# Performance work log

Hardware: AMD Instinct MI355X
Metric: run time of the kernel (lower is better)

Reference implementation:

```python
import jax, jax.numpy as jnp
import numpy as np

N_NODES = 15
K = 5
L_IN = 1920
C_OUT = 256
L3 = L_IN - 3 * K + 3  # 1908
EPS = 1e-5


def setup_inputs() -> dict:
    key = jax.random.key(0)
    ks = jax.random.split(key, 18)
    B, E = 128, 56
    s = 0.05
    inp = {
        'X': jax.random.normal(ks[0], (B, N_NODES, L_IN), jnp.float32),
        'edge_index': jax.random.randint(ks[1], (2, E), 0, N_NODES),
        'edge_weight': jax.random.uniform(ks[2], (E,), jnp.float32),
        # grouped conv params (groups = N_NODES): per-group channels 1->16->32->1
        'conv1_w': jax.random.normal(ks[3], (16 * N_NODES, 1, K), jnp.float32) * s,
        'conv1_b': jnp.zeros((16 * N_NODES,), jnp.float32),
        'conv2_w': jax.random.normal(ks[4], (32 * N_NODES, 16, K), jnp.float32) * s,
        'conv2_b': jnp.zeros((32 * N_NODES,), jnp.float32),
        'conv3_w': jax.random.normal(ks[5], (N_NODES, 32, K), jnp.float32) * s,
        'conv3_b': jnp.zeros((N_NODES,), jnp.float32),
        # GCNConv: lin weight [out,in] + bias
        'gcn_w': jax.random.normal(ks[6], (C_OUT, L3), jnp.float32) * s,
        'gcn_b': jnp.zeros((C_OUT,), jnp.float32),
        'lin1_w': jax.random.normal(ks[7], (C_OUT, L_IN), jnp.float32) * s,
        'lin1_b': jnp.zeros((C_OUT,), jnp.float32),
        # GraphNorm params
        'gn_w': jnp.ones((C_OUT,), jnp.float32),
        'gn_b': jnp.zeros((C_OUT,), jnp.float32),
        'gn_ms': jnp.ones((C_OUT,), jnp.float32),
        'out_w': jax.random.normal(ks[8], (16, C_OUT), jnp.float32) * s,
        'out_b': jnp.zeros((16,), jnp.float32),
    }
    return inp


def _gconv(x, w, b):
    # grouped valid conv1d, NCH layout
    y = jax.lax.conv_general_dilated(
        x, w, window_strides=(1,), padding='VALID',
        dimension_numbers=('NCH', 'OIH', 'NCH'),
        feature_group_count=N_NODES)
    return y + b[None, :, None]


def _gcn(x, edge_index, edge_weight, W, b):
    # x: [B, N, L3]; batched GCNConv with shared edge structure (no per-t loop)
    src, dst = edge_index[0], edge_index[1]
    loop = jnp.arange(N_NODES)
    src = jnp.concatenate([src, loop])
    dst = jnp.concatenate([dst, loop])
    ew = jnp.concatenate([edge_weight, jnp.ones((N_NODES,), edge_weight.dtype)])
    deg = jnp.zeros((N_NODES,), ew.dtype).at[dst].add(ew)  # in-degree on target
    dinv = jnp.where(deg > 0, jax.lax.rsqrt(deg), 0.0)
    norm = dinv[src] * ew * dinv[dst]  # [E']
    xl = jnp.einsum('bnf,of->bno', x, W)  # [B, N, C_OUT]
    msg = norm[None, :, None] * xl[:, src, :]  # [B, E', C_OUT]
    out = jnp.zeros_like(xl).at[:, dst, :].add(msg)
    return out + b


def reference(X, edge_index, edge_weight, conv1_w, conv1_b, conv2_w, conv2_b,
              conv3_w, conv3_b, gcn_w, gcn_b, lin1_w, lin1_b, gn_w, gn_b,
              gn_ms, out_w, out_b):
    h = jax.nn.leaky_relu(_gconv(X, conv1_w, conv1_b), 0.01)
    h = jax.nn.leaky_relu(_gconv(h, conv2_w, conv2_b), 0.01)
    h = jax.nn.leaky_relu(_gconv(h, conv3_w, conv3_b), 0.01)  # [B, N, L3]
    T = _gcn(h, edge_index, edge_weight, gcn_w, gcn_b)  # [B, N, C_OUT]
    # GraphNorm with batch=None -> single graph over dim 0
    mean = T.mean(axis=0, keepdims=True)
    out = T - mean * gn_ms
    var = (out * out).mean(axis=0, keepdims=True)
    T = gn_w * out / jnp.sqrt(var + EPS) + gn_b
    T = jax.nn.elu(T + jnp.einsum('bnl,ol->bno', X, lin1_w) + lin1_b)
    output = T.mean(axis=1)  # global_mean_pool over nodes -> [B, C_OUT]
    class_output = output @ out_w.T + out_b  # [B, 16]
    return (output, class_output)
```

## Files before the change

kernel.cpp:

```cpp
#include <hip/hip_runtime.h>

typedef unsigned short u16;
typedef unsigned int   u32;

typedef short shortx8   __attribute__((ext_vector_type(8)));
typedef float floatx4   __attribute__((ext_vector_type(4)));
typedef float floatx16  __attribute__((ext_vector_type(16)));
typedef u32   uintx4    __attribute__((ext_vector_type(4)));

typedef u32     u32a     __attribute__((may_alias));
typedef uintx4  uintx4a  __attribute__((may_alias));
typedef shortx8 shortx8a __attribute__((may_alias));

__device__ __forceinline__ u16 f2bf(float f){
  union { float f; u32 i; } v; v.f = f;
  return (u16)((v.i + 0x7fffu + ((v.i >> 16) & 1u)) >> 16);
}
__device__ __forceinline__ u16 f2bf_fast(float f){
  union { float f; u32 i; } v; v.f = f;
  return (u16)((v.i + 0x8000u) >> 16);
}
__device__ __forceinline__ u32 pack2(float lo, float hi){
  union { float f; u32 i; } a, b; a.f = lo; b.f = hi;
  return __builtin_amdgcn_perm(b.i + 0x8000u, a.i + 0x8000u, 0x07060302u);
}
__device__ __forceinline__ u32 cvtpk2(float lo, float hi){
#if __has_builtin(__builtin_amdgcn_cvt_pk_bf16_f32)
  auto pv = __builtin_amdgcn_cvt_pk_bf16_f32(lo, hi);
  if constexpr (sizeof(pv) == 4){
    u32 out; __builtin_memcpy(&out, &pv, 4); return out;
  } else {
    return pack2(lo, hi);
  }
#else
  return pack2(lo, hi);
#endif
}
__device__ __forceinline__ float lrelu(float v){ return fmaxf(v, 0.01f*v); }

__global__ void __launch_bounds__(512, 4) fused_conv(
    const float* __restrict__ X,
    const float* __restrict__ w1, const float* __restrict__ b1,
    const float* __restrict__ w2, const float* __restrict__ b2,
    const float* __restrict__ w3, const float* __restrict__ b3,
    u16* __restrict__ h3p, u16* __restrict__ Xb,
    const float* __restrict__ lw, u16* __restrict__ lwb,
    const float* __restrict__ gw, u16* __restrict__ gwp){
  const int tid  = threadIdx.x;
  const int node = blockIdx.z;
  const int p    = blockIdx.x * 60;
  const int b0   = blockIdx.y * 16;

  __shared__ __attribute__((aligned(16))) u16 sH1[8*1632];
  __shared__ __attribute__((aligned(16))) u16 sH2[8*2720];
  __shared__ __attribute__((aligned(16))) u16 sW2f[2560];
  __shared__ __attribute__((aligned(16))) u16 sW3f[160];
  __shared__ u16 sXb[16*76];
  __shared__ float sW1[80], sB1[16], sB2[32];

  {
    const int bid = blockIdx.x + 32*(blockIdx.y + 8*blockIdx.z);
    if (tid < 256){
      int gid = bid*256 + tid;
      if (gid < 491520){
        lwb[gid] = f2bf(lw[gid]);
      } else {
        int g2 = gid - 491520;
        int row = g2 / 1920;
        int col = g2 - row*1920;
        gwp[g2] = (col < 1908) ? f2bf(gw[row*1908 + col]) : (u16)0;
      }
    }
  }

  {
    const int bls = tid >> 5, i0 = tid & 31;
    const float* xrow = X  + (size_t)((b0 + bls)*15 + node)*1920;
    u16*        xbrow = Xb + (size_t)((b0 + bls)*15 + node)*1920;
    #pragma unroll
    for (int u = 0; u < 3; ++u){
      int i = i0 + 32*u;
      if (i < 76){
        int g = p + i;
        float xv = (i < 72 && g < 1920) ? xrow[g] : 0.f;
        u16 xb = f2bf_fast(xv);
        sXb[bls*76 + i] = xb;
        if (i < 60) xbrow[g] = xb;
      }
    }
    #pragma unroll
    for (int u = 0; u < 5; ++u){
      int d = tid + 512*u;
      int j = d & 7, oc = (d >> 3) & 31, h = (d >> 8) & 1, tap = d >> 9;
      sW2f[d] = f2bf(w2[node*2560 + (oc*16 + h*8 + j)*5 + tap]);
    }
    if (tid < 160){
      int icc = tid / 5, tp = tid - 5*icc;
      sW3f[tp*32 + icc] = f2bf(w3[node*160 + tid]);
    }
    if (tid < 80) sW1[tid] = w1[node*80 + tid];
    if (tid < 16) sB1[tid] = b1[node*16 + tid];
    if (tid < 32) sB2[tid] = b2[node*32 + tid];
  }
  __syncthreads();

  const int w = tid >> 6, lane = tid & 63;
  const int m = lane & 15, quad = lane >> 4;
  const int t32 = lane & 31, h = lane >> 5;

  shortx8 a2t[5];
  #pragma unroll
  for (int tap = 0; tap < 5; ++tap)
    a2t[tap] = *(const shortx8a*)&sW2f[((tap*2 + h)*32 + t32)*8];

  float biasr[16];
  #pragma unroll
  for (int r = 0; r < 16; ++r)
    biasr[r] = sB2[(r&3) + 8*(r>>2) + 4*h];

  shortx8 a3[5];
  {
    const shortx8 zv = {0,0,0,0,0,0,0,0};
    #pragma unroll
    for (int tp = 0; tp < 5; ++tp){
      shortx8 t = *(const shortx8a*)&sW3f[tp*32 + quad*8];
      a3[tp] = (m == 0) ? t : zv;
    }
  }
  const float b3v = b3[node];

  u16* h1w = sH1 + w*1632;
  u16* h2w = sH2 + w*2720;
  for (int i = lane; i < 160; i += 64) h2w[2560 + i] = 0;

  const int c1ic = (lane & 7)*2, c1t0 = (lane >> 3)*9;
  float wa[5], wb[5];
  #pragma unroll
  for (int k = 0; k < 5; ++k){ wa[k] = sW1[c1ic*5 + k]; wb[k] = sW1[c1ic*5 + 5 + k]; }
  const float ba = sB1[c1ic], bbv = sB1[c1ic + 1];

  for (int bb = 0; bb < 2; ++bb){
    const int bl = w + bb*8;

    {
      const u16* xr = sXb + bl*76;
      union { u32 i; float f; } cv;
      float xw[5];
      #pragma unroll
      for (int k = 0; k < 4; ++k){ cv.i = ((u32)xr[c1t0+k]) << 16; xw[k] = cv.f; }
      #pragma unroll
      for (int i = 0; i < 9; ++i){
        const int t = c1t0 + i;
        cv.i = ((u32)xr[t + 4]) << 16; xw[4] = cv.f;
        float va = ba  + wa[0]*xw[0] + wa[1]*xw[1] + wa[2]*xw[2] + wa[3]*xw[3] + wa[4]*xw[4];
        float vb = bbv + wb[0]*xw[0] + wb[1]*xw[1] + wb[2]*xw[2] + wb[3]*xw[3] + wb[4]*xw[4];
        va = lrelu(va); vb = lrelu(vb);
        if (t < 68) *(u32a*)(h1w + t*24 + c1ic) = cvtpk2(va, vb);
        xw[0] = xw[1]; xw[1] = xw[2]; xw[2] = xw[3]; xw[3] = xw[4];
      }
    }
    __syncthreads();

    #pragma unroll
    for (int nt = 0; nt < 2; ++nt){
      const int t0 = nt*32;
      floatx16 acc;
      #pragma unroll
      for (int r = 0; r < 16; ++r) acc[r] = biasr[r];
      #pragma unroll
      for (int tap = 0; tap < 5; ++tap){
        shortx8 bfr = *(const shortx8a*)(h1w + (t0 + t32 + tap)*24 + h*8);
        acc = __builtin_amdgcn_mfma_f32_32x32x16_bf16(a2t[tap], bfr, acc, 0, 0, 0);
      }
      u16* dst = h2w + (t0 + t32)*40;
      #pragma unroll
      for (int r = 0; r < 16; r += 2){
        float v0 = lrelu(acc[r]);
        float v1 = lrelu(acc[r+1]);
        const int oc0 = (r&3) + 8*(r>>2) + 4*h;
        *(u32a*)(dst + oc0) = cvtpk2(v0, v1);
      }
    }
    __syncthreads();

    const int rg = (b0 + bl)*15 + node;
    #pragma unroll
    for (int nt = 0; nt < 4; ++nt){
      floatx4 acc3 = {0.f,0.f,0.f,0.f};
      if (lane < 16) acc3[0] = b3v;
      #pragma unroll
      for (int tp = 0; tp < 5; ++tp){
        shortx8 bfr = *(const shortx8a*)(h2w + (nt*16 + m + tp)*40 + quad*8);
        acc3 = __builtin_amdgcn_mfma_f32_16x16x32_bf16(a3[tp], bfr, acc3, 0, 0, 0);
      }
      const int tl = nt*16 + lane;
      if (lane < 16 && tl < 60){
        const int t3 = p + tl;
        float v = lrelu(acc3[0]);
        h3p[(size_t)rg*1920 + t3] = (t3 < 1908) ? f2bf_fast(v) : (u16)0;
      }
    }
  }
}

__global__ void __launch_bounds__(256) gemm_nt(
    const u16* __restrict__ A0, const u16* __restrict__ B0, float* __restrict__ O0,
    const u16* __restrict__ A1, const u16* __restrict__ B1, float* __restrict__ O1,
    float* __restrict__ gZ){
  const int job = blockIdx.z;
  const u16* A; const u16* Bm; float* O;
  if (job == 0){ A = A0; Bm = B0; O = O0; } else { A = A1; Bm = B1; O = O1; }
  __shared__ __attribute__((aligned(16))) u16 sA[64*88];
  __shared__ __attribute__((aligned(16))) u16 sB[64*88];
  const int tid = threadIdx.x;
  if (blockIdx.x == 0 && blockIdx.y == 0 && job == 0){
    #pragma unroll
    for (int u = 0; u < 30; ++u) gZ[tid + 256*u] = 0.f;
  }
  const int m0 = blockIdx.x*64, n0 = blockIdx.y*64;
  const int row = tid >> 2, kc = tid & 3;
  const int w = tid >> 6, lane = tid & 63;
  const int m = lane & 15, quad = lane >> 4;
  const int mo = (w & 1)*32, no = (w >> 1)*32;
  floatx4 acc[2][2];
  #pragma unroll
  for (int i = 0; i < 2; ++i)
    #pragma unroll
    for (int j = 0; j < 2; ++j)
      #pragma unroll
      for (int r = 0; r < 4; ++r) acc[i][j][r] = 0.f;

  const u16* ap = A  + (size_t)(m0 + row)*1920 + kc*8;
  const u16* bp = Bm + (size_t)(n0 + row)*1920 + kc*8;
  for (int kt = 0; kt < 30; ++kt){
    uintx4 va0 = *(const uintx4a*)ap;
    uintx4 va1 = *(const uintx4a*)(ap + 32);
    uintx4 vb0 = *(const uintx4a*)bp;
    uintx4 vb1 = *(const uintx4a*)(bp + 32);
    ap += 64; bp += 64;
    *(uintx4a*)&sA[row*88 + kc*8]      = va0;
    *(uintx4a*)&sA[row*88 + 32 + kc*8] = va1;
    *(uintx4a*)&sB[row*88 + kc*8]      = vb0;
    *(uintx4a*)&sB[row*88 + 32 + kc*8] = vb1;
    __syncthreads();
    #pragma unroll
    for (int ks = 0; ks < 64; ks += 32){
      const shortx8 af0 = *(const shortx8a*)&sA[(mo      + m)*88 + ks + quad*8];
      const shortx8 af1 = *(const shortx8a*)&sA[(mo + 16 + m)*88 + ks + quad*8];
      const shortx8 bf0 = *(const shortx8a*)&sB[(no      + m)*88 + ks + quad*8];
      const shortx8 bf1 = *(const shortx8a*)&sB[(no + 16 + m)*88 + ks + quad*8];
      acc[0][0] = __builtin_amdgcn_mfma_f32_16x16x32_bf16(af0, bf0, acc[0][0], 0, 0, 0);
      acc[0][1] = __builtin_amdgcn_mfma_f32_16x16x32_bf16(af0, bf1, acc[0][1], 0, 0, 0);
      acc[1][0] = __builtin_amdgcn_mfma_f32_16x16x32_bf16(af1, bf0, acc[1][0], 0, 0, 0);
      acc[1][1] = __builtin_amdgcn_mfma_f32_16x16x32_bf16(af1, bf1, acc[1][1], 0, 0, 0);
    }
    __syncthreads();
  }
  #pragma unroll
  for (int mi = 0; mi < 2; ++mi)
    #pragma unroll
    for (int ni = 0; ni < 2; ++ni)
      #pragma unroll
      for (int r = 0; r < 4; ++r){
        int rr = m0 + mo + mi*16 + quad*4 + r;
        int cc = n0 + no + ni*16 + m;
        O[(size_t)rr*256 + cc] = acc[mi][ni][r];
      }
}

__global__ void __launch_bounds__(256) gcn_agg(
    const float* __restrict__ xl, const int* __restrict__ ei,
    const float* __restrict__ ew, const float* __restrict__ gcn_b,
    float* __restrict__ Tpre, float* __restrict__ gS, float* __restrict__ gS2){
  const int b = blockIdx.x, tid = threadIdx.x;
  __shared__ float sxl[15*256];
  __shared__ float s_deg[15], s_dinv[15], s_norm[71];
  __shared__ int   s_cnt[15], s_start[16], s_fill[15], s_srcl[71];
  if (tid < 15){ s_deg[tid] = 0.f; s_cnt[tid] = 0; s_fill[tid] = 0; }
  #pragma unroll
  for (int n = 0; n < 15; ++n)
    sxl[n*256 + tid] = xl[(size_t)(b*15 + n)*256 + tid];
  __syncthreads();
  int se = 0, de = 0; float we = 0.f;
  if (tid < 71){
    if (tid < 56){ se = ei[tid]; de = ei[56 + tid]; we = ew[tid]; }
    else         { se = tid - 56; de = tid - 56; we = 1.0f; }
    atomicAdd(&s_deg[de], we);
    atomicAdd(&s_cnt[de], 1);
  }
  __syncthreads();
  if (tid < 15) s_dinv[tid] = s_deg[tid] > 0.f ? rsqrtf(s_deg[tid]) : 0.f;
  if (tid == 0){
    int a = 0;
    for (int n = 0; n < 15; ++n){ s_start[n] = a; a += s_cnt[n]; }
    s_start[15] = a;
  }
  __syncthreads();
  if (tid < 71){
    float nrm = s_dinv[se]*we*s_dinv[de];
    int pos = s_start[de] + atomicAdd(&s_fill[de], 1);
    s_srcl[pos] = se; s_norm[pos] = nrm;
  }
  __syncthreads();
  const float gb = gcn_b[tid];
  for (int n = 0; n < 15; ++n){
    float acc = gb;
    const int e0 = s_start[n], e1 = s_start[n+1];
    for (int idx = e0; idx < e1; ++idx)
      acc += s_norm[idx]*sxl[s_srcl[idx]*256 + tid];
    Tpre[(size_t)(b*15 + n)*256 + tid] = acc;
    atomicAdd(&gS [n*256 + tid], acc);
    atomicAdd(&gS2[n*256 + tid], acc*acc);
  }
}

__global__ void __launch_bounds__(256) finalize_k(
    const float* __restrict__ Tpre, const float* __restrict__ l1,
    const float* __restrict__ gS, const float* __restrict__ gS2,
    const float* __restrict__ gn_ms, const float* __restrict__ gn_w,
    const float* __restrict__ gn_b, const float* __restrict__ lin1_b,
    const float* __restrict__ out_w, const float* __restrict__ out_b,
    float* __restrict__ dout){
  const int b = blockIdx.x, tid = threadIdx.x;
  __shared__ float spool[256], spart[256];
  const float gnb = gn_b[tid], lb = lin1_b[tid];
  const float gms = gn_ms[tid], gwc = gn_w[tid];
  float acc = 0.f;
  #pragma unroll
  for (int n = 0; n < 15; ++n){
    const float s  = gS [n*256 + tid];
    const float s2 = gS2[n*256 + tid];
    const float mean = s*(1.f/128.f);
    const float mo   = mean*gms;
    float var = s2*(1.f/128.f) - 2.f*mo*mean + mo*mo;
    var = fmaxf(var, 0.f);
    const float scal = gwc*rsqrtf(var + 1e-5f);
    float t = (Tpre[(size_t)(b*15 + n)*256 + tid] - mo)*scal
              + gnb + l1[(size_t)(b*15 + n)*256 + tid] + lb;
    t = t > 0.f ? t : (__expf(t) - 1.f);
    acc += t;
  }
  const float pool = acc*(1.f/15.f);
  dout[b*256 + tid] = pool;
  spool[tid] = pool;
  __syncthreads();
  const int j = tid >> 4, q = tid & 15;
  float s = 0.f;
  for (int i = 0; i < 16; ++i){
    int cc = q + i*16;
    s += spool[cc]*out_w[j*256 + cc];
  }
  spart[tid] = s;
  __syncthreads();
  if (tid < 16){
    float tot = out_b[tid];
    #pragma unroll
    for (int i = 0; i < 16; ++i) tot += spart[tid*16 + i];
    dout[32768 + b*16 + tid] = tot;
  }
}

extern "C" void kernel_launch(void* const* d_in, const int* in_sizes, int n_in,
                              void* d_out, int out_size, void* d_ws, size_t ws_size,
                              hipStream_t stream){
  (void)in_sizes; (void)n_in; (void)out_size; (void)ws_size;
  const float* X    = (const float*)d_in[0];
  const int*   ei   = (const int*)d_in[1];
  const float* ew   = (const float*)d_in[2];
  const float* w1   = (const float*)d_in[3];
  const float* b1   = (const float*)d_in[4];
  const float* w2   = (const float*)d_in[5];
  const float* b2   = (const float*)d_in[6];
  const float* w3   = (const float*)d_in[7];
  const float* b3   = (const float*)d_in[8];
  const float* gw   = (const float*)d_in[9];
  const float* gb   = (const float*)d_in[10];
  const float* lw   = (const float*)d_in[11];
  const float* lb   = (const float*)d_in[12];
  const float* gnw  = (const float*)d_in[13];
  const float* gnb  = (const float*)d_in[14];
  const float* gnms = (const float*)d_in[15];
  const float* ow   = (const float*)d_in[16];
  const float* ob   = (const float*)d_in[17];

  char* ws = (char*)d_ws;
  u16*   h3p  = (u16*)(ws + 0);
  u16*   gwp  = (u16*)(ws + 7372800);
  u16*   Xb   = (u16*)(ws + 8355840);
  u16*   lwb  = (u16*)(ws + 15728640);
  float* xl   = (float*)(ws + 16711680);
  float* l1   = (float*)(ws + 18677760);
  float* gS   = (float*)(ws + 20643840);
  float* gS2  = (float*)(ws + 20659200);
  float* Tpre = (float*)(ws + 0);

  fused_conv<<<dim3(32, 8, 15), dim3(512), 0, stream>>>(X, w1, b1, w2, b2, w3, b3,
                                                        h3p, Xb, lw, lwb, gw, gwp);
  gemm_nt   <<<dim3(30, 4, 2),  dim3(256), 0, stream>>>(Xb, lwb, l1, h3p, gwp, xl, gS);
  gcn_agg   <<<dim3(128),       dim3(256), 0, stream>>>(xl, ei, ew, gb, Tpre, gS, gS2);
  finalize_k<<<dim3(128),       dim3(256), 0, stream>>>(Tpre, l1, gS, gS2,
                                                        gnms, gnw, gnb, lb, ow, ob,
                                                        (float*)d_out);
}
```

Before: 205.5 us.

## Pair waves per batch row to halve shared scratch and raise occupancy

```diff
diff --git a/kernel.cpp b/kernel.cpp
--- a/kernel.cpp
+++ b/kernel.cpp
@@ -38,7 +38,7 @@
 }
 __device__ __forceinline__ float lrelu(float v){ return fmaxf(v, 0.01f*v); }
 
-__global__ void __launch_bounds__(512, 4) fused_conv(
+__global__ void __launch_bounds__(512, 6) fused_conv(
     const float* __restrict__ X,
     const float* __restrict__ w1, const float* __restrict__ b1,
     const float* __restrict__ w2, const float* __restrict__ b2,
@@ -51,8 +51,8 @@
   const int p    = blockIdx.x * 60;
   const int b0   = blockIdx.y * 16;
 
-  __shared__ __attribute__((aligned(16))) u16 sH1[8*1632];
-  __shared__ __attribute__((aligned(16))) u16 sH2[8*2720];
+  __shared__ __attribute__((aligned(16))) u16 sH1[4*1632];
+  __shared__ __attribute__((aligned(16))) u16 sH2[4*2720];
   __shared__ __attribute__((aligned(16))) u16 sW2f[2560];
   __shared__ __attribute__((aligned(16))) u16 sW3f[160];
   __shared__ u16 sXb[16*76];
@@ -91,8 +91,8 @@
     #pragma unroll
     for (int u = 0; u < 5; ++u){
       int d = tid + 512*u;
-      int j = d & 7, oc = (d >> 3) & 31, h = (d >> 8) & 1, tap = d >> 9;
-      sW2f[d] = f2bf(w2[node*2560 + (oc*16 + h*8 + j)*5 + tap]);
+      int j = d & 7, oc = (d >> 3) & 31, kh = (d >> 8) & 1, tap = d >> 9;
+      sW2f[d] = f2bf(w2[node*2560 + (oc*16 + kh*8 + j)*5 + tap]);
     }
     if (tid < 160){
       int icc = tid / 5, tp = tid - 5*icc;
@@ -105,18 +105,19 @@
   __syncthreads();
 
   const int w = tid >> 6, lane = tid & 63;
+  const int pw = w >> 1, ph = w & 1;
   const int m = lane & 15, quad = lane >> 4;
-  const int t32 = lane & 31, h = lane >> 5;
+  const int t32 = lane & 31, kh = lane >> 5;
 
   shortx8 a2t[5];
   #pragma unroll
   for (int tap = 0; tap < 5; ++tap)
-    a2t[tap] = *(const shortx8a*)&sW2f[((tap*2 + h)*32 + t32)*8];
+    a2t[tap] = *(const shortx8a*)&sW2f[((tap*2 + kh)*32 + t32)*8];
 
   float biasr[16];
   #pragma unroll
   for (int r = 0; r < 16; ++r)
-    biasr[r] = sB2[(r&3) + 8*(r>>2) + 4*h];
+    biasr[r] = sB2[(r&3) + 8*(r>>2) + 4*kh];
 
   shortx8 a3[5];
   {
@@ -129,28 +130,30 @@
   }
   const float b3v = b3[node];
 
-  u16* h1w = sH1 + w*1632;
-  u16* h2w = sH2 + w*2720;
-  for (int i = lane; i < 160; i += 64) h2w[2560 + i] = 0;
-
-  const int c1ic = (lane & 7)*2, c1t0 = (lane >> 3)*9;
+  u16* h1w = sH1 + pw*1632;
+  u16* h2w = sH2 + pw*2720;
+  for (int i = lane + ph*64; i < 160; i += 128) h2w[2560 + i] = 0;
+
+  const int c1ic = (lane & 7)*2;
+  const int cc   = (lane >> 3) + ph*8;
+  const int t0c  = cc*5;
   float wa[5], wb[5];
   #pragma unroll
   for (int k = 0; k < 5; ++k){ wa[k] = sW1[c1ic*5 + k]; wb[k] = sW1[c1ic*5 + 5 + k]; }
   const float ba = sB1[c1ic], bbv = sB1[c1ic + 1];
 
-  for (int bb = 0; bb < 2; ++bb){
-    const int bl = w + bb*8;
-
-    {
+  for (int bb = 0; bb < 4; ++bb){
+    const int bl = pw + bb*4;
+
+    if (t0c < 68){
       const u16* xr = sXb + bl*76;
       union { u32 i; float f; } cv;
       float xw[5];
       #pragma unroll
-      for (int k = 0; k < 4; ++k){ cv.i = ((u32)xr[c1t0+k]) << 16; xw[k] = cv.f; }
-      #pragma unroll
-      for (int i = 0; i < 9; ++i){
-        const int t = c1t0 + i;
+      for (int k = 0; k < 4; ++k){ cv.i = ((u32)xr[t0c+k]) << 16; xw[k] = cv.f; }
+      #pragma unroll
+      for (int i = 0; i < 5; ++i){
+        const int t = t0c + i;
         cv.i = ((u32)xr[t + 4]) << 16; xw[4] = cv.f;
         float va = ba  + wa[0]*xw[0] + wa[1]*xw[1] + wa[2]*xw[2] + wa[3]*xw[3] + wa[4]*xw[4];
         float vb = bbv + wb[0]*xw[0] + wb[1]*xw[1] + wb[2]*xw[2] + wb[3]*xw[3] + wb[4]*xw[4];
@@ -161,15 +164,14 @@
     }
     __syncthreads();
 
-    #pragma unroll
-    for (int nt = 0; nt < 2; ++nt){
-      const int t0 = nt*32;
+    {
+      const int t0 = ph*32;
       floatx16 acc;
       #pragma unroll
       for (int r = 0; r < 16; ++r) acc[r] = biasr[r];
       #pragma unroll
       for (int tap = 0; tap < 5; ++tap){
-        shortx8 bfr = *(const shortx8a*)(h1w + (t0 + t32 + tap)*24 + h*8);
+        shortx8 bfr = *(const shortx8a*)(h1w + (t0 + t32 + tap)*24 + kh*8);
         acc = __builtin_amdgcn_mfma_f32_32x32x16_bf16(a2t[tap], bfr, acc, 0, 0, 0);
       }
       u16* dst = h2w + (t0 + t32)*40;
@@ -177,7 +179,7 @@
       for (int r = 0; r < 16; r += 2){
         float v0 = lrelu(acc[r]);
         float v1 = lrelu(acc[r+1]);
-        const int oc0 = (r&3) + 8*(r>>2) + 4*h;
+        const int oc0 = (r&3) + 8*(r>>2) + 4*kh;
         *(u32a*)(dst + oc0) = cvtpk2(v0, v1);
       }
     }
@@ -185,7 +187,8 @@
 
     const int rg = (b0 + bl)*15 + node;
     #pragma unroll
-    for (int nt = 0; nt < 4; ++nt){
+    for (int i = 0; i < 2; ++i){
+      const int nt = 2*ph + i;
       floatx4 acc3 = {0.f,0.f,0.f,0.f};
       if (lane < 16) acc3[0] = b3v;
       #pragma unroll
```

Measured after the change: 406.3 us. +97.7%, slower.
